# Optimization experiments

Hardware: AMD Instinct MI355X
Metric: run time of the kernel (lower is better)

## Reference

```python
import jax, jax.numpy as jnp
import numpy as np

TEMPERATURE = 1.0  # registered buffer in the torch module
SOFTPLUS_SHIFT = 0.5413


def setup_inputs() -> dict:
    key = jax.random.key(0)
    k0, k1, k2, k3 = jax.random.split(key, 4)
    B, S, Din, Dout, T, DEP, H = 4, 2048, 1024, 512, 12, 3, 3
    L = 2 ** DEP
    return {
        "x": jax.random.normal(k0, (B, S, Din), jnp.float32),
        # normal(0, 0.1) init as in _init_forest_params
        "decision_weights": 0.1 * jax.random.normal(k1, (T, DEP, Din), jnp.float32),
        "decision_biases": jnp.zeros((T, DEP), jnp.float32),
        "node_temperature_logits": jnp.zeros((T, DEP), jnp.float32),
        "gate_w": jax.random.normal(k2, (T, Din), jnp.float32) / np.sqrt(Din),
        "gate_b": jnp.zeros((T,), jnp.float32),
        # xavier_normal over trailing (L, Dout) matrices
        "leaf_outputs": jax.random.normal(k3, (H, T, L, Dout), jnp.float32) * np.sqrt(2.0 / (L + Dout)),
    }


def _leaf_probs_depth3(decisions):
    # decisions: (B, S, T, 3) sigmoid routing probs; Kronecker product over 3 levels -> 8 leaves
    d0, d1, d2 = decisions[..., 0], decisions[..., 1], decisions[..., 2]
    p0 = jnp.stack([d0, 1.0 - d0], axis=-1)  # (B,S,T,2)
    p1 = jnp.stack([d1, 1.0 - d1], axis=-1)
    p2 = jnp.stack([d2, 1.0 - d2], axis=-1)
    B, S, T, _ = p0.shape
    lp = p0[..., :, None, None] * p1[..., None, :, None] * p2[..., None, None, :]
    return lp.reshape(B, S, T, 8)


def reference(x, decision_weights, decision_biases, node_temperature_logits, gate_w, gate_b, leaf_outputs):
    # decision logits per tree/level: (B,S,T,DEP)
    dec = jnp.einsum('bsd,tnd->bstn', x, decision_weights) + decision_biases
    node_temps = TEMPERATURE * jax.nn.softplus(node_temperature_logits + SOFTPLUS_SHIFT)  # (T,DEP)
    dec = jax.nn.sigmoid(dec / node_temps)
    leaf_probs = _leaf_probs_depth3(dec)  # (B,S,T,L)
    weights = jax.nn.softmax(x @ gate_w.T + gate_b, axis=-1)  # (B,S,T)
    # fused form of: per_tree = einsum('bstl,htld->hbstd'); out = einsum('hbstd,bst->hbsd')
    out = jnp.einsum('bstl,bst,htld->hbsd', leaf_probs, weights, leaf_outputs)
    # original returns list of per-head outputs; return stacked (H,B,S,Dout)
    return out
```

## Files before the change

kernel.cpp:

```cpp
#include <hip/hip_runtime.h>
#include <math.h>

#define NROWS 8192
#define DIN   1024
#define NT    12
#define NDEP  3
#define NDEC  36
#define NCOL  48
#define NC    96
#define NH    3
#define DOUT  512
#define CLP   104

typedef short bf16x8 __attribute__((ext_vector_type(8)));
typedef float f32x4  __attribute__((ext_vector_type(4)));

__device__ inline unsigned short f2bf(float f) {
    unsigned u = __float_as_uint(f);
    u = u + 0x7fff + ((u >> 16) & 1);
    return (unsigned short)(u >> 16);
}
__device__ inline float bf2f(unsigned short h) {
    return __uint_as_float(((unsigned)h) << 16);
}
__device__ inline unsigned cvt_pk(float a, float b) {
    unsigned r;
    asm("v_cvt_pk_bf16_f32 %0, %1, %2" : "=v"(r) : "v"(a), "v"(b));
    return r;
}
__device__ inline void split8(const float4 a, const float4 b, bf16x8& hi, bf16x8& lo) {
    union U { unsigned u[4]; bf16x8 v; };
    U H, L;
    H.u[0] = cvt_pk(a.x, a.y); H.u[1] = cvt_pk(a.z, a.w);
    H.u[2] = cvt_pk(b.x, b.y); H.u[3] = cvt_pk(b.z, b.w);
    const float r0 = a.x - __uint_as_float(H.u[0] << 16);
    const float r1 = a.y - __uint_as_float(H.u[0] & 0xffff0000u);
    const float r2 = a.z - __uint_as_float(H.u[1] << 16);
    const float r3 = a.w - __uint_as_float(H.u[1] & 0xffff0000u);
    const float r4 = b.x - __uint_as_float(H.u[2] << 16);
    const float r5 = b.y - __uint_as_float(H.u[2] & 0xffff0000u);
    const float r6 = b.z - __uint_as_float(H.u[3] << 16);
    const float r7 = b.w - __uint_as_float(H.u[3] & 0xffff0000u);
    L.u[0] = cvt_pk(r0, r1); L.u[1] = cvt_pk(r2, r3);
    L.u[2] = cvt_pk(r4, r5); L.u[3] = cvt_pk(r6, r7);
    hi = H.v; lo = L.v;
}

__global__ __launch_bounds__(256) void k_prep(const float* __restrict__ dw,
                                              const float* __restrict__ gw,
                                              const float* __restrict__ db,
                                              const float* __restrict__ ntl,
                                              const float* __restrict__ leaf,
                                              unsigned short* __restrict__ w_hi,
                                              unsigned short* __restrict__ w_lo,
                                              unsigned short* __restrict__ leafT,
                                              float* __restrict__ it_zb) {
    const int b = blockIdx.x;
    if (b < 192) {
        const int i = b * 256 + threadIdx.x;
        const int n = i >> 10;
        const float v = (n < NDEC) ? dw[i] : gw[i - NDEC * DIN];
        const unsigned short h = f2bf(v);
        w_hi[i] = h;
        w_lo[i] = f2bf(v - bf2f(h));
    } else if (b < 264) {
        const int i  = (b - 192) * 256 + threadIdx.x;
        const int hq = i % (NH * DOUT);
        const int kq = i / (NH * DOUT);
        const int h  = hq >> 9, d = hq & 511;
        bf16x8 v;
#pragma unroll
        for (int e = 0; e < 8; ++e)
            v[e] = (short)f2bf(leaf[(size_t)(h * NC + kq * 8 + e) * DOUT + d]);
        *(bf16x8*)(leafT + (size_t)hq * NC + kq * 8) = v;
    } else {
        const int i = threadIdx.x;
        if (i < NDEC) {
            const float v  = ntl[i] + 0.5413f;
            const float sp = (v > 20.0f) ? v : logf(1.0f + expf(v));
            const float it = 1.0f / sp;
            it_zb[i]        = it;
            it_zb[NDEC + i] = db[i] * it;
        }
    }
}

__global__ __launch_bounds__(256) void k_fused(const float* __restrict__ x,
                                               const unsigned short* __restrict__ w_hi,
                                               const unsigned short* __restrict__ w_lo,
                                               const unsigned short* __restrict__ leafT,
                                               const float* __restrict__ it_zb,
                                               const float* __restrict__ gb,
                                               float* __restrict__ out) {
    __shared__ float Lred[4][NCOL][17];
    __shared__ __align__(16) unsigned short Cl[16][CLP];

    const int tid  = threadIdx.x;
    const int wv   = tid >> 6, lane = tid & 63;
    const int m    = lane & 15;
    const int kq   = lane >> 4;
    const int row0 = blockIdx.x * 16;

    f32x4 acc[3];
#pragma unroll
    for (int nf = 0; nf < 3; ++nf)
#pragma unroll
        for (int r = 0; r < 4; ++r) acc[nf][r] = 0.0f;

    const float*          xp  = x    + (size_t)(row0 + m) * DIN + wv * 256 + kq * 8;
    const unsigned short* whp = w_hi + (size_t)m * DIN + wv * 256 + kq * 8;
    const unsigned short* wlp = w_lo + (size_t)m * DIN + wv * 256 + kq * 8;

#pragma unroll
    for (int ks = 0; ks < 8; ++ks) {
        const float4 xa = *(const float4*)(xp + ks * 32);
        const float4 xb = *(const float4*)(xp + ks * 32 + 4);
        bf16x8 xhi, xlo;
        split8(xa, xb, xhi, xlo);
#pragma unroll
        for (int nf = 0; nf < 3; ++nf) {
            const bf16x8 whi = *(const bf16x8*)(whp + (size_t)nf * 16 * DIN + ks * 32);
            const bf16x8 wlo = *(const bf16x8*)(wlp + (size_t)nf * 16 * DIN + ks * 32);
            acc[nf] = __builtin_amdgcn_mfma_f32_16x16x32_bf16(xhi, whi, acc[nf], 0, 0, 0);
            acc[nf] = __builtin_amdgcn_mfma_f32_16x16x32_bf16(xlo, whi, acc[nf], 0, 0, 0);
            acc[nf] = __builtin_amdgcn_mfma_f32_16x16x32_bf16(xhi, wlo, acc[nf], 0, 0, 0);
        }
    }
#pragma unroll
    for (int nf = 0; nf < 3; ++nf)
#pragma unroll
        for (int r = 0; r < 4; ++r)
            Lred[wv][nf * 16 + m][kq * 4 + r] = acc[nf][r];
    __syncthreads();

    {
        const int erow = tid >> 4;
        const int slot = tid & 15;
        float lg0 = 0.f, lg1 = 0.f, lg2 = 0.f, g = -1e30f;
        if (slot < NT) {
            float lgg = 0.f;
#pragma unroll
            for (int w = 0; w < 4; ++w) {
                lg0 += Lred[w][slot * 3 + 0][erow];
                lg1 += Lred[w][slot * 3 + 1][erow];
                lg2 += Lred[w][slot * 3 + 2][erow];
                lgg += Lred[w][NDEC + slot][erow];
            }
            g = lgg + gb[slot];
        }
        float mx = g;
#pragma unroll
        for (int off = 1; off < 16; off <<= 1) mx = fmaxf(mx, __shfl_xor(mx, off, 16));
        const float e = (slot < NT) ? expf(g - mx) : 0.f;
        float s = e;
#pragma unroll
        for (int off = 1; off < 16; off <<= 1) s += __shfl_xor(s, off, 16);
        if (slot < NT) {
            const float wt = e * __builtin_amdgcn_rcpf(s);
            const float z0 = lg0 * it_zb[slot * 3 + 0] + it_zb[NDEC + slot * 3 + 0];
            const float z1 = lg1 * it_zb[slot * 3 + 1] + it_zb[NDEC + slot * 3 + 1];
            const float z2 = lg2 * it_zb[slot * 3 + 2] + it_zb[NDEC + slot * 3 + 2];
            const float d0 = __builtin_amdgcn_rcpf(1.0f + expf(-z0));
            const float d1 = __builtin_amdgcn_rcpf(1.0f + expf(-z1));
            const float d2 = __builtin_amdgcn_rcpf(1.0f + expf(-z2));
            float c[8];
#pragma unroll
            for (int l = 0; l < 8; ++l) {
                const float p0 = (l & 4) ? (1.0f - d0) : d0;
                const float p1 = (l & 2) ? (1.0f - d1) : d1;
                const float p2 = (l & 1) ? (1.0f - d2) : d2;
                c[l] = wt * p0 * p1 * p2;
            }
            union { unsigned u[4]; bf16x8 v; } P;
            P.u[0] = cvt_pk(c[0], c[1]); P.u[1] = cvt_pk(c[2], c[3]);
            P.u[2] = cvt_pk(c[4], c[5]); P.u[3] = cvt_pk(c[6], c[7]);
            *(bf16x8*)&Cl[erow][slot * 8] = P.v;
        }
    }
    __syncthreads();

    bf16x8 afr[3];
#pragma unroll
    for (int ks = 0; ks < 3; ++ks)
        afr[ks] = *(const bf16x8*)&Cl[m][ks * 32 + kq * 8];

#pragma unroll
    for (int i = 0; i < 24; ++i) {
        const int f   = wv * 24 + i;
        const int h   = f >> 5;
        const int d0c = (f & 31) * 16;
        const unsigned short* bp = leafT + ((size_t)h * DOUT + d0c + m) * NC + kq * 8;
        f32x4 a;
#pragma unroll
        for (int r = 0; r < 4; ++r) a[r] = 0.0f;
#pragma unroll
        for (int ks = 0; ks < 3; ++ks) {
            const bf16x8 bfr = *(const bf16x8*)(bp + ks * 32);
            a = __builtin_amdgcn_mfma_f32_16x16x32_bf16(afr[ks], bfr, a, 0, 0, 0);
        }
        float* op = out + ((size_t)h * NROWS + row0 + kq * 4) * DOUT + d0c + m;
#pragma unroll
        for (int r = 0; r < 4; ++r) op[(size_t)r * DOUT] = a[r];
    }
}

extern "C" void kernel_launch(void* const* d_in, const int* in_sizes, int n_in,
                              void* d_out, int out_size, void* d_ws, size_t ws_size,
                              hipStream_t stream) {
    const float* x    = (const float*)d_in[0];
    const float* dw   = (const float*)d_in[1];
    const float* db   = (const float*)d_in[2];
    const float* ntl  = (const float*)d_in[3];
    const float* gw   = (const float*)d_in[4];
    const float* gb   = (const float*)d_in[5];
    const float* leaf = (const float*)d_in[6];
    float* out = (float*)d_out;

    char* ws = (char*)d_ws;
    unsigned short* w_hi  = (unsigned short*)(ws);
    unsigned short* w_lo  = (unsigned short*)(ws + 98304);
    unsigned short* leafT = (unsigned short*)(ws + 196608);
    float*          it_zb = (float*)(ws + 491520);

    k_prep<<<265, 256, 0, stream>>>(dw, gw, db, ntl, leaf, w_hi, w_lo, leafT, it_zb);
    k_fused<<<NROWS / 16, 256, 0, stream>>>(x, w_hi, w_lo, leafT, it_zb, gb, out);
}
```

Measured before the change: 39.17 us.

## Use 8 waves per block and transpose MFMA operands for vector stores

Doubles the block to 512 threads so the K-split of the routing GEMM spans 8 waves and each wave emits half as many leaf-output tiles. The MFMA operands are swapped so each lane's accumulator holds 4 consecutive columns of one row. That allows float4 writes to LDS and coalesced 16-byte global output stores in place of strided scalar stores. The cost is a deeper LDS reduction over 8 partials and half the threads sitting idle during the softmax/sigmoid stage.

```diff
diff --git a/kernel.cpp b/kernel.cpp
--- a/kernel.cpp
+++ b/kernel.cpp
@@ -11,6 +11,7 @@
 #define NH    3
 #define DOUT  512
 #define CLP   104
+#define LRP   52
 
 typedef short bf16x8 __attribute__((ext_vector_type(8)));
 typedef float f32x4  __attribute__((ext_vector_type(4)));
@@ -85,14 +86,14 @@
     }
 }
 
-__global__ __launch_bounds__(256) void k_fused(const float* __restrict__ x,
+__global__ __launch_bounds__(512) void k_fused(const float* __restrict__ x,
                                                const unsigned short* __restrict__ w_hi,
                                                const unsigned short* __restrict__ w_lo,
                                                const unsigned short* __restrict__ leafT,
                                                const float* __restrict__ it_zb,
                                                const float* __restrict__ gb,
                                                float* __restrict__ out) {
-    __shared__ float Lred[4][NCOL][17];
+    __shared__ __align__(16) float Lred[8][16][LRP];
     __shared__ __align__(16) unsigned short Cl[16][CLP];
 
     const int tid  = threadIdx.x;
@@ -107,12 +108,12 @@
 #pragma unroll
         for (int r = 0; r < 4; ++r) acc[nf][r] = 0.0f;
 
-    const float*          xp  = x    + (size_t)(row0 + m) * DIN + wv * 256 + kq * 8;
-    const unsigned short* whp = w_hi + (size_t)m * DIN + wv * 256 + kq * 8;
-    const unsigned short* wlp = w_lo + (size_t)m * DIN + wv * 256 + kq * 8;
-
-#pragma unroll
-    for (int ks = 0; ks < 8; ++ks) {
+    const float*          xp  = x    + (size_t)(row0 + m) * DIN + wv * 128 + kq * 8;
+    const unsigned short* whp = w_hi + (size_t)m * DIN + wv * 128 + kq * 8;
+    const unsigned short* wlp = w_lo + (size_t)m * DIN + wv * 128 + kq * 8;
+
+#pragma unroll
+    for (int ks = 0; ks < 4; ++ks) {
         const float4 xa = *(const float4*)(xp + ks * 32);
         const float4 xb = *(const float4*)(xp + ks * 32 + 4);
         bf16x8 xhi, xlo;
@@ -121,30 +122,28 @@
         for (int nf = 0; nf < 3; ++nf) {
             const bf16x8 whi = *(const bf16x8*)(whp + (size_t)nf * 16 * DIN + ks * 32);
             const bf16x8 wlo = *(const bf16x8*)(wlp + (size_t)nf * 16 * DIN + ks * 32);
-            acc[nf] = __builtin_amdgcn_mfma_f32_16x16x32_bf16(xhi, whi, acc[nf], 0, 0, 0);
-            acc[nf] = __builtin_amdgcn_mfma_f32_16x16x32_bf16(xlo, whi, acc[nf], 0, 0, 0);
-            acc[nf] = __builtin_amdgcn_mfma_f32_16x16x32_bf16(xhi, wlo, acc[nf], 0, 0, 0);
+            acc[nf] = __builtin_amdgcn_mfma_f32_16x16x32_bf16(whi, xhi, acc[nf], 0, 0, 0);
+            acc[nf] = __builtin_amdgcn_mfma_f32_16x16x32_bf16(whi, xlo, acc[nf], 0, 0, 0);
+            acc[nf] = __builtin_amdgcn_mfma_f32_16x16x32_bf16(wlo, xhi, acc[nf], 0, 0, 0);
         }
     }
 #pragma unroll
     for (int nf = 0; nf < 3; ++nf)
-#pragma unroll
-        for (int r = 0; r < 4; ++r)
-            Lred[wv][nf * 16 + m][kq * 4 + r] = acc[nf][r];
+        *(f32x4*)&Lred[wv][m][nf * 16 + kq * 4] = acc[nf];
     __syncthreads();
 
-    {
+    if (tid < 256) {
         const int erow = tid >> 4;
         const int slot = tid & 15;
         float lg0 = 0.f, lg1 = 0.f, lg2 = 0.f, g = -1e30f;
         if (slot < NT) {
             float lgg = 0.f;
 #pragma unroll
-            for (int w = 0; w < 4; ++w) {
-                lg0 += Lred[w][slot * 3 + 0][erow];
-                lg1 += Lred[w][slot * 3 + 1][erow];
-                lg2 += Lred[w][slot * 3 + 2][erow];
-                lgg += Lred[w][NDEC + slot][erow];
+            for (int w = 0; w < 8; ++w) {
+                lg0 += Lred[w][erow][slot * 3 + 0];
+                lg1 += Lred[w][erow][slot * 3 + 1];
+                lg2 += Lred[w][erow][slot * 3 + 2];
+                lgg += Lred[w][erow][NDEC + slot];
             }
             g = lgg + gb[slot];
         }
@@ -179,14 +178,14 @@
     }
     __syncthreads();
 
-    bf16x8 afr[3];
+    bf16x8 cfr[3];
 #pragma unroll
     for (int ks = 0; ks < 3; ++ks)
-        afr[ks] = *(const bf16x8*)&Cl[m][ks * 32 + kq * 8];
-
-#pragma unroll
-    for (int i = 0; i < 24; ++i) {
-        const int f   = wv * 24 + i;
+        cfr[ks] = *(const bf16x8*)&Cl[m][ks * 32 + kq * 8];
+
+#pragma unroll
+    for (int i = 0; i < 12; ++i) {
+        const int f   = wv * 12 + i;
         const int h   = f >> 5;
         const int d0c = (f & 31) * 16;
         const unsigned short* bp = leafT + ((size_t)h * DOUT + d0c + m) * NC + kq * 8;
@@ -195,12 +194,10 @@
         for (int r = 0; r < 4; ++r) a[r] = 0.0f;
 #pragma unroll
         for (int ks = 0; ks < 3; ++ks) {
-            const bf16x8 bfr = *(const bf16x8*)(bp + ks * 32);
-            a = __builtin_amdgcn_mfma_f32_16x16x32_bf16(afr[ks], bfr, a, 0, 0, 0);
-        }
-        float* op = out + ((size_t)h * NROWS + row0 + kq * 4) * DOUT + d0c + m;
-#pragma unroll
-        for (int r = 0; r < 4; ++r) op[(size_t)r * DOUT] = a[r];
+            const bf16x8 lfr = *(const bf16x8*)(bp + ks * 32);
+            a = __builtin_amdgcn_mfma_f32_16x16x32_bf16(lfr, cfr[ks], a, 0, 0, 0);
+        }
+        *(f32x4*)(out + ((size_t)h * NROWS + row0 + m) * DOUT + d0c + kq * 4) = a;
     }
 }
 
@@ -223,5 +220,5 @@
     float*          it_zb = (float*)(ws + 491520);
 
     k_prep<<<265, 256, 0, stream>>>(dw, gw, db, ntl, leaf, w_hi, w_lo, leafT, it_zb);
-    k_fused<<<NROWS / 16, 256, 0, stream>>>(x, w_hi, w_lo, leafT, it_zb, gb, out);
-}
+    k_fused<<<NROWS / 16, 512, 0, stream>>>(x, w_hi, w_lo, leafT, it_zb, gb, out);
+}
```

Result: slower. 42.76 us (+9.2%).
